# Kernel tuning notes

Measured on AMD Instinct MI355X. Metric: run time of the kernel, lower is better.

The kernel has to match this reference:

```python
import jax, jax.numpy as jnp
import numpy as np

S, D, DD, REL, R = 4096, 128, 64, 8, 512
FC_IN = DD * (REL * S + R)  # 2,129,920


def setup_inputs() -> dict:
    key = jax.random.key(0)
    ks = jax.random.split(key, 7)
    return {
        "inputs": jax.random.randint(ks[0], (S,), 0, 2, dtype=jnp.int32),
        "rule_features": jax.random.normal(ks[1], (DD, R), dtype=jnp.float32),
        "embed_w": jax.random.normal(ks[2], (S, D), dtype=jnp.float32),
        "rel_w": jax.random.normal(ks[3], (REL, D), dtype=jnp.float32),
        "dise_w": jax.random.normal(ks[4], (DD, D), dtype=jnp.float32),
        "fc_w": jax.random.normal(ks[5], (DD, FC_IN), dtype=jnp.float32) * 0.01,
        "fc_b": jax.random.normal(ks[6], (DD,), dtype=jnp.float32),
    }


def reference(inputs, rule_features, embed_w, rel_w, dise_w, fc_w, fc_b):
    eps = 1e-6
    dt = embed_w.dtype
    # mask rows where the symptom indicator is nonzero (original builds mask
    # row-by-row with torch.nonzero; equivalent to broadcasting inputs != 0)
    mask = (inputs != 0).astype(dt)                                  # [S]
    # (embed + rel) * mask  -> [S, REL, D] -> [S*REL, D]
    x = (embed_w[:, None, :] + rel_w[None, :, :]) * mask[:, None, None]
    x = x.reshape(-1, embed_w.shape[-1])                             # [N, D]
    # cosine similarity of every disease embedding vs every (sym,rel) vector
    sq = jnp.sum(x * x, axis=1)                                      # [N]
    xn = jnp.where(sq > 0, jnp.sqrt(jnp.where(sq > 0, sq, 1.0)), 0.0)
    dn = jnp.sqrt(jnp.sum(dise_w * dise_w, axis=1))                  # [DD]
    dots = jnp.einsum('kd,nd->kn', dise_w, x)                        # [DD, N]
    kg = dots / jnp.maximum(dn[:, None] * xn[None, :], eps)          # [DD, N]
    hidden = jnp.concatenate([rule_features, kg], axis=1).reshape(1, -1)
    out = jax.nn.sigmoid(hidden @ fc_w.T + fc_b)                     # [1, DD]
    return out
```

## Files before the change

### kernel.cpp

```cpp
#include <hip/hip_runtime.h>
#include <math.h>

namespace {
constexpr int S_N   = 4096;
constexpr int D_N   = 128;
constexpr int DD_N  = 64;
constexpr int REL_N = 8;
constexpr int R_N   = 512;
constexpr int NTOT  = S_N * REL_N;
constexpr int ROWLEN = R_N + NTOT;
constexpr long long FC_IN_N = (long long)DD_N * ROWLEN;
constexpr int NCH   = 32;
constexpr int CHUNK2 = (int)(FC_IN_N / NCH);
constexpr int NF4   = CHUNK2 / 4;
constexpr int RPB   = 8;
constexpr int KG_N  = DD_N / RPB;
constexpr int NBLK3 = NCH * KG_N;
constexpr int SEP   = 132;
typedef float floatx4 __attribute__((ext_vector_type(4)));

__device__ __forceinline__ float dot4(const float4& a, const float4& b) {
    return a.x*b.x + a.y*b.y + a.z*b.z + a.w*b.w;
}
}

__global__ __launch_bounds__(256) void k_pre(const int* __restrict__ inputs,
                                             const float* __restrict__ dise,
                                             const float* __restrict__ embed,
                                             const float* __restrict__ rel,
                                             float* __restrict__ DE,
                                             float* __restrict__ DR,
                                             float* __restrict__ dsc_g,
                                             float* __restrict__ xinv) {
    __shared__ float sd[DD_N * 129];
    __shared__ __align__(16) float se[16 * SEP];
    __shared__ __align__(16) float sr[REL_N * SEP];
    __shared__ float rr[REL_N];
    const int tid  = threadIdx.x;
    const int lane = tid & 63;
    const int wave = tid >> 6;
    const int s0   = blockIdx.x * 16;

    for (int i = tid; i < DD_N * D_N; i += 256)
        sd[(i >> 7) * 129 + (i & 127)] = dise[i];
    for (int i = tid; i < 16 * 32; i += 256) {
        const int row = i >> 5, col = i & 31;
        *reinterpret_cast<float4*>(&se[row * SEP + col * 4]) =
            reinterpret_cast<const float4*>(embed + (size_t)s0 * D_N)[i];
    }
    if (tid < REL_N * 32) {
        const int row = tid >> 5, col = tid & 31;
        *reinterpret_cast<float4*>(&sr[row * SEP + col * 4]) =
            reinterpret_cast<const float4*>(rel)[tid];
    }
    __syncthreads();

    if (tid < REL_N) {
        float a = 0.f;
        for (int e = 0; e < D_N; ++e) { float v = sr[tid * SEP + e]; a += v * v; }
        rr[tid] = a;
    }

    float dw[D_N];
    float dsq = 0.f;
    #pragma unroll
    for (int e = 0; e < D_N; ++e) {
        dw[e] = sd[lane * 129 + e];
        dsq += dw[e] * dw[e];
    }
    const float dsc = rsqrtf(dsq);

    if (blockIdx.x == 0) {
        if (wave == 0) dsc_g[lane] = dsc;
        #pragma unroll
        for (int rr2 = 0; rr2 < 2; ++rr2) {
            const int r = wave * 2 + rr2;
            float a = 0.f;
            #pragma unroll
            for (int e = 0; e < D_N; ++e) a += dw[e] * sr[r * SEP + e];
            DR[lane * REL_N + r] = a;
        }
    }

    {
        float4 o;
        float* op = reinterpret_cast<float*>(&o);
        #pragma unroll
        for (int jj = 0; jj < 4; ++jj) {
            const int nl = wave * 4 + jj;
            const float4* xr = reinterpret_cast<const float4*>(&se[nl * SEP]);
            float a0 = 0.f, a1 = 0.f, a2 = 0.f, a3 = 0.f;
            #pragma unroll
            for (int i = 0; i < 32; i += 4) {
                float4 x0 = xr[i], x1 = xr[i + 1], x2 = xr[i + 2], x3 = xr[i + 3];
                a0 += dw[4*i+ 0]*x0.x + dw[4*i+ 1]*x0.y + dw[4*i+ 2]*x0.z + dw[4*i+ 3]*x0.w;
                a1 += dw[4*i+ 4]*x1.x + dw[4*i+ 5]*x1.y + dw[4*i+ 6]*x1.z + dw[4*i+ 7]*x1.w;
                a2 += dw[4*i+ 8]*x2.x + dw[4*i+ 9]*x2.y + dw[4*i+10]*x2.z + dw[4*i+11]*x2.w;
                a3 += dw[4*i+12]*x3.x + dw[4*i+13]*x3.y + dw[4*i+14]*x3.z + dw[4*i+15]*x3.w;
            }
            op[jj] = a0 + a1 + a2 + a3;
        }
        *reinterpret_cast<float4*>(DE + (size_t)lane * S_N + s0 + wave * 4) = o;
    }

    __syncthreads();

    if (tid < 128) {
        const int sl = tid >> 3, r = tid & 7;
        const float4* ev4 = reinterpret_cast<const float4*>(&se[sl * SEP]);
        const float4* rv4 = reinterpret_cast<const float4*>(&sr[r * SEP]);
        float ee = 0.f, er = 0.f;
        #pragma unroll
        for (int i = 0; i < 32; ++i) {
            float4 ev = ev4[i], rv = rv4[i];
            ee += dot4(ev, ev);
            er += dot4(ev, rv);
        }
        const float sq = ee + 2.f * er + rr[r];
        const bool m = (inputs[s0 + sl] != 0);
        xinv[(size_t)(s0 + sl) * REL_N + r] = (m && sq > 0.f) ? rsqrtf(sq) : 0.f;
    }
}

__global__ __launch_bounds__(256) void k_kg2(const float* __restrict__ rf,
                                             const float* __restrict__ DE,
                                             const float* __restrict__ DR,
                                             const float* __restrict__ dsc_g,
                                             const float* __restrict__ xinv,
                                             float* __restrict__ h) {
    __shared__ __align__(16) float sx[8192];
    __shared__ float sD[1024];
    const int tid = threadIdx.x;
    const int dd  = blockIdx.x >> 2;
    const int q   = blockIdx.x & 3;
    const int n0  = q * 8192;
    const int s0  = q * 1024;

    for (int i = tid; i < 2048; i += 256)
        reinterpret_cast<float4*>(sx)[i] = reinterpret_cast<const float4*>(xinv + n0)[i];
    if (tid < 256)
        reinterpret_cast<float4*>(sD)[tid] =
            reinterpret_cast<const float4*>(DE + (size_t)dd * S_N + s0)[tid];
    const float dsc = dsc_g[dd];
    const float4 drlo = reinterpret_cast<const float4*>(DR + dd * REL_N)[0];
    const float4 drhi = reinterpret_cast<const float4*>(DR + dd * REL_N)[1];
    const float4 drv = (tid & 1) ? drhi : drlo;
    __syncthreads();

    float* hb = h + (size_t)dd * ROWLEN + R_N + n0;
    #pragma unroll
    for (int i = 0; i < 8; ++i) {
        const int f4i = i * 256 + tid;
        const int ln  = f4i * 4;
        const float de = sD[f4i >> 1];
        float4 xv = reinterpret_cast<const float4*>(sx)[f4i];
        float4 o;
        o.x = dsc * xv.x * (de + drv.x);
        o.y = dsc * xv.y * (de + drv.y);
        o.z = dsc * xv.z * (de + drv.z);
        o.w = dsc * xv.w * (de + drv.w);
        *reinterpret_cast<float4*>(hb + ln) = o;
    }
    if (q == 0 && tid < 128)
        reinterpret_cast<float4*>(h + (size_t)dd * ROWLEN)[tid] =
            reinterpret_cast<const float4*>(rf + (size_t)dd * R_N)[tid];
}

__global__ __launch_bounds__(512, 1) void k_mv(const float* __restrict__ fcw,
                                               const float* __restrict__ h,
                                               float* __restrict__ partials) {
    const int tid = threadIdx.x;
    const int swz = (blockIdx.x & 7) * (NBLK3 / 8) + (blockIdx.x >> 3);
    const int c  = swz >> 3;
    const int kg = swz & 7;

    const float4* hp = reinterpret_cast<const float4*>(h) + (size_t)c * NF4;
    const floatx4* wp = reinterpret_cast<const floatx4*>(fcw)
                        + (size_t)(kg * RPB) * (FC_IN_N / 4) + (size_t)c * NF4;

    float acc[RPB];
    #pragma unroll
    for (int j = 0; j < RPB; ++j) acc[j] = 0.f;

    #pragma unroll 2
    for (int i = 0; i < 32; ++i) {
        const int idx = i * 512 + tid;
        float4 hv = hp[idx];
        #pragma unroll
        for (int j = 0; j < RPB; ++j) {
            floatx4 w = __builtin_nontemporal_load(wp + (size_t)j * (FC_IN_N / 4) + idx);
            acc[j] += w.x * hv.x + w.y * hv.y + w.z * hv.z + w.w * hv.w;
        }
    }
    if (tid < 256) {
        const int idx = 32 * 512 + tid;
        float4 hv = hp[idx];
        #pragma unroll
        for (int j = 0; j < RPB; ++j) {
            floatx4 w = __builtin_nontemporal_load(wp + (size_t)j * (FC_IN_N / 4) + idx);
            acc[j] += w.x * hv.x + w.y * hv.y + w.z * hv.z + w.w * hv.w;
        }
    }

    #pragma unroll
    for (int m = 32; m >= 1; m >>= 1) {
        #pragma unroll
        for (int j = 0; j < RPB; ++j) acc[j] += __shfl_xor(acc[j], m);
    }
    __shared__ float red[8][RPB];
    if ((tid & 63) == 0) {
        const int wv = tid >> 6;
        #pragma unroll
        for (int j = 0; j < RPB; ++j) red[wv][j] = acc[j];
    }
    __syncthreads();
    if (tid < RPB) {
        float s = 0.f;
        #pragma unroll
        for (int wv = 0; wv < 8; ++wv) s += red[wv][tid];
        partials[(size_t)swz * RPB + tid] = s;
    }
}

__global__ __launch_bounds__(256) void k_fin(const float* __restrict__ partials,
                                             const float* __restrict__ fcb,
                                             float* __restrict__ out) {
    const int tid = threadIdx.x;
    const int k = tid & 63, g = tid >> 6;
    float s = 0.f;
    for (int b = g; b < NCH; b += 4) s += partials[(size_t)b * 64 + k];
    __shared__ float red[4][64];
    red[g][k] = s;
    __syncthreads();
    if (tid < 64) {
        float t = red[0][tid] + red[1][tid] + red[2][tid] + red[3][tid] + fcb[tid];
        out[tid] = 1.0f / (1.0f + expf(-t));
    }
}

extern "C" void kernel_launch(void* const* d_in, const int* in_sizes, int n_in,
                              void* d_out, int out_size, void* d_ws, size_t ws_size,
                              hipStream_t stream) {
    const int*   inputs = (const int*)  d_in[0];
    const float* rf     = (const float*)d_in[1];
    const float* embed  = (const float*)d_in[2];
    const float* rel    = (const float*)d_in[3];
    const float* dise   = (const float*)d_in[4];
    const float* fcw    = (const float*)d_in[5];
    const float* fcb    = (const float*)d_in[6];
    float* out = (float*)d_out;

    float* ws = (float*)d_ws;
    float* h        = ws;
    float* partials = h + FC_IN_N;
    float* DE       = partials + NCH * 64;
    float* DR       = DE + (size_t)DD_N * S_N;
    float* dsc_g    = DR + DD_N * REL_N;
    float* xinv     = dsc_g + 64;

    hipLaunchKernelGGL(k_pre,  dim3(S_N / 16), dim3(256), 0, stream,
                       inputs, dise, embed, rel, DE, DR, dsc_g, xinv);
    hipLaunchKernelGGL(k_kg2,  dim3(DD_N * 4), dim3(256), 0, stream, rf, DE, DR, dsc_g, xinv, h);
    hipLaunchKernelGGL(k_mv,   dim3(NBLK3),    dim3(512), 0, stream, fcw, h, partials);
    hipLaunchKernelGGL(k_fin,  dim3(1),        dim3(256), 0, stream, partials, fcb, out);
}
```

Before: 112.1 us.

## Fuse final reduction into matvec via last-block atomic counter; drop nontemporal loads

Removes the separate single-block finalize kernel. Each matvec block now writes its partials, fences, and bumps a global counter, and the last block to finish sums the partials, adds the bias and applies the sigmoid. The counter is reset in the first kernel. The fc weight loads also switch from nontemporal builtins to plain float4 loads, which changes cache behaviour on the dominant weight stream. The goal is to save one kernel launch, at the cost of an atomic and fences in every block.

After: 134.7 us, median of 2. 1.2x slower.

```diff
diff --git a/kernel.cpp b/kernel.cpp
--- a/kernel.cpp
+++ b/kernel.cpp
@@ -31,7 +31,8 @@
                                              float* __restrict__ DE,
                                              float* __restrict__ DR,
                                              float* __restrict__ dsc_g,
-                                             float* __restrict__ xinv) {
+                                             float* __restrict__ xinv,
+                                             int* __restrict__ counter) {
     __shared__ float sd[DD_N * 129];
     __shared__ __align__(16) float se[16 * SEP];
     __shared__ __align__(16) float sr[REL_N * SEP];
@@ -40,6 +41,8 @@
     const int lane = tid & 63;
     const int wave = tid >> 6;
     const int s0   = blockIdx.x * 16;
+
+    if (blockIdx.x == 0 && tid == 0) *counter = 0;
 
     for (int i = tid; i < DD_N * D_N; i += 256)
         sd[(i >> 7) * 129 + (i & 127)] = dise[i];
@@ -168,14 +171,17 @@
 
 __global__ __launch_bounds__(512, 1) void k_mv(const float* __restrict__ fcw,
                                                const float* __restrict__ h,
-                                               float* __restrict__ partials) {
+                                               float* __restrict__ partials,
+                                               const float* __restrict__ fcb,
+                                               float* __restrict__ out,
+                                               int* __restrict__ counter) {
     const int tid = threadIdx.x;
     const int swz = (blockIdx.x & 7) * (NBLK3 / 8) + (blockIdx.x >> 3);
     const int c  = swz >> 3;
     const int kg = swz & 7;
 
     const float4* hp = reinterpret_cast<const float4*>(h) + (size_t)c * NF4;
-    const floatx4* wp = reinterpret_cast<const floatx4*>(fcw)
+    const float4* wp = reinterpret_cast<const float4*>(fcw)
                         + (size_t)(kg * RPB) * (FC_IN_N / 4) + (size_t)c * NF4;
 
     float acc[RPB];
@@ -188,7 +194,7 @@
         float4 hv = hp[idx];
         #pragma unroll
         for (int j = 0; j < RPB; ++j) {
-            floatx4 w = __builtin_nontemporal_load(wp + (size_t)j * (FC_IN_N / 4) + idx);
+            float4 w = wp[(size_t)j * (FC_IN_N / 4) + idx];
             acc[j] += w.x * hv.x + w.y * hv.y + w.z * hv.z + w.w * hv.w;
         }
     }
@@ -197,7 +203,7 @@
         float4 hv = hp[idx];
         #pragma unroll
         for (int j = 0; j < RPB; ++j) {
-            floatx4 w = __builtin_nontemporal_load(wp + (size_t)j * (FC_IN_N / 4) + idx);
+            float4 w = wp[(size_t)j * (FC_IN_N / 4) + idx];
             acc[j] += w.x * hv.x + w.y * hv.y + w.z * hv.z + w.w * hv.w;
         }
     }
@@ -214,27 +220,28 @@
         for (int j = 0; j < RPB; ++j) red[wv][j] = acc[j];
     }
     __syncthreads();
-    if (tid < RPB) {
-        float s = 0.f;
-        #pragma unroll
-        for (int wv = 0; wv < 8; ++wv) s += red[wv][tid];
-        partials[(size_t)swz * RPB + tid] = s;
-    }
-}
-
-__global__ __launch_bounds__(256) void k_fin(const float* __restrict__ partials,
-                                             const float* __restrict__ fcb,
-                                             float* __restrict__ out) {
-    const int tid = threadIdx.x;
-    const int k = tid & 63, g = tid >> 6;
-    float s = 0.f;
-    for (int b = g; b < NCH; b += 4) s += partials[(size_t)b * 64 + k];
-    __shared__ float red[4][64];
-    red[g][k] = s;
-    __syncthreads();
-    if (tid < 64) {
-        float t = red[0][tid] + red[1][tid] + red[2][tid] + red[3][tid] + fcb[tid];
-        out[tid] = 1.0f / (1.0f + expf(-t));
+
+    __shared__ bool amLast;
+    if (tid == 0) {
+        #pragma unroll
+        for (int j = 0; j < RPB; ++j) {
+            float s = 0.f;
+            #pragma unroll
+            for (int wv = 0; wv < 8; ++wv) s += red[wv][j];
+            partials[(size_t)swz * RPB + j] = s;
+        }
+        __threadfence();
+        amLast = (atomicAdd(counter, 1) == NBLK3 - 1);
+    }
+    __syncthreads();
+
+    if (amLast) {
+        __threadfence();
+        if (tid < DD_N) {
+            float t = fcb[tid];
+            for (int cc = 0; cc < NCH; ++cc) t += partials[(size_t)cc * DD_N + tid];
+            out[tid] = 1.0f / (1.0f + expf(-t));
+        }
     }
 }
 
@@ -257,10 +264,11 @@
     float* DR       = DE + (size_t)DD_N * S_N;
     float* dsc_g    = DR + DD_N * REL_N;
     float* xinv     = dsc_g + 64;
+    int*   counter  = (int*)(xinv + NTOT);
 
     hipLaunchKernelGGL(k_pre,  dim3(S_N / 16), dim3(256), 0, stream,
-                       inputs, dise, embed, rel, DE, DR, dsc_g, xinv);
+                       inputs, dise, embed, rel, DE, DR, dsc_g, xinv, counter);
     hipLaunchKernelGGL(k_kg2,  dim3(DD_N * 4), dim3(256), 0, stream, rf, DE, DR, dsc_g, xinv, h);
-    hipLaunchKernelGGL(k_mv,   dim3(NBLK3),    dim3(512), 0, stream, fcw, h, partials);
-    hipLaunchKernelGGL(k_fin,  dim3(1),        dim3(256), 0, stream, partials, fcb, out);
-}
+    hipLaunchKernelGGL(k_mv,   dim3(NBLK3),    dim3(512), 0, stream,
+                       fcw, h, partials, fcb, out, counter);
+}
```

## Fuse hidden-vector construction into the matvec kernel and drop the h buffer

Applied to the files above, without the earlier changes.

Removes the k_kg2 kernel that materialized the 2.1M-float hidden vector h in workspace. k_mv now rebuilds each hidden chunk on the fly from rule_features, DE, DR, dsc and xinv while streaming fc_w, with each chunk covering exactly two disease rows. This saves the write and re-read of about 8.5MB plus one kernel launch. In exchange, the hidden values are recomputed by all 8 row-group blocks that share a chunk, which adds ALU work and small cached reads inside the bandwidth-bound loop.

Result: faster. 103.6 us (-7.5%).

```diff
diff --git a/kernel.cpp b/kernel.cpp
--- a/kernel.cpp
+++ b/kernel.cpp
@@ -122,83 +122,62 @@
     }
 }
 
-__global__ __launch_bounds__(256) void k_kg2(const float* __restrict__ rf,
-                                             const float* __restrict__ DE,
-                                             const float* __restrict__ DR,
-                                             const float* __restrict__ dsc_g,
-                                             const float* __restrict__ xinv,
-                                             float* __restrict__ h) {
-    __shared__ __align__(16) float sx[8192];
-    __shared__ float sD[1024];
-    const int tid = threadIdx.x;
-    const int dd  = blockIdx.x >> 2;
-    const int q   = blockIdx.x & 3;
-    const int n0  = q * 8192;
-    const int s0  = q * 1024;
-
-    for (int i = tid; i < 2048; i += 256)
-        reinterpret_cast<float4*>(sx)[i] = reinterpret_cast<const float4*>(xinv + n0)[i];
-    if (tid < 256)
-        reinterpret_cast<float4*>(sD)[tid] =
-            reinterpret_cast<const float4*>(DE + (size_t)dd * S_N + s0)[tid];
-    const float dsc = dsc_g[dd];
-    const float4 drlo = reinterpret_cast<const float4*>(DR + dd * REL_N)[0];
-    const float4 drhi = reinterpret_cast<const float4*>(DR + dd * REL_N)[1];
-    const float4 drv = (tid & 1) ? drhi : drlo;
-    __syncthreads();
-
-    float* hb = h + (size_t)dd * ROWLEN + R_N + n0;
-    #pragma unroll
-    for (int i = 0; i < 8; ++i) {
-        const int f4i = i * 256 + tid;
-        const int ln  = f4i * 4;
-        const float de = sD[f4i >> 1];
-        float4 xv = reinterpret_cast<const float4*>(sx)[f4i];
-        float4 o;
-        o.x = dsc * xv.x * (de + drv.x);
-        o.y = dsc * xv.y * (de + drv.y);
-        o.z = dsc * xv.z * (de + drv.z);
-        o.w = dsc * xv.w * (de + drv.w);
-        *reinterpret_cast<float4*>(hb + ln) = o;
-    }
-    if (q == 0 && tid < 128)
-        reinterpret_cast<float4*>(h + (size_t)dd * ROWLEN)[tid] =
-            reinterpret_cast<const float4*>(rf + (size_t)dd * R_N)[tid];
-}
-
 __global__ __launch_bounds__(512, 1) void k_mv(const float* __restrict__ fcw,
-                                               const float* __restrict__ h,
+                                               const float* __restrict__ rf,
+                                               const float* __restrict__ DE,
+                                               const float* __restrict__ DR,
+                                               const float* __restrict__ dsc_g,
+                                               const float* __restrict__ xinv,
                                                float* __restrict__ partials) {
     const int tid = threadIdx.x;
     const int swz = (blockIdx.x & 7) * (NBLK3 / 8) + (blockIdx.x >> 3);
     const int c  = swz >> 3;
     const int kg = swz & 7;
 
-    const float4* hp = reinterpret_cast<const float4*>(h) + (size_t)c * NF4;
     const floatx4* wp = reinterpret_cast<const floatx4*>(fcw)
                         + (size_t)(kg * RPB) * (FC_IN_N / 4) + (size_t)c * NF4;
+    const float4* xv4 = reinterpret_cast<const float4*>(xinv);
 
     float acc[RPB];
     #pragma unroll
     for (int j = 0; j < RPB; ++j) acc[j] = 0.f;
 
-    #pragma unroll 2
-    for (int i = 0; i < 32; ++i) {
-        const int idx = i * 512 + tid;
-        float4 hv = hp[idx];
-        #pragma unroll
-        for (int j = 0; j < RPB; ++j) {
-            floatx4 w = __builtin_nontemporal_load(wp + (size_t)j * (FC_IN_N / 4) + idx);
-            acc[j] += w.x * hv.x + w.y * hv.y + w.z * hv.z + w.w * hv.w;
-        }
-    }
-    if (tid < 256) {
-        const int idx = 32 * 512 + tid;
-        float4 hv = hp[idx];
-        #pragma unroll
-        for (int j = 0; j < RPB; ++j) {
-            floatx4 w = __builtin_nontemporal_load(wp + (size_t)j * (FC_IN_N / 4) + idx);
-            acc[j] += w.x * hv.x + w.y * hv.y + w.z * hv.z + w.w * hv.w;
+    #pragma unroll
+    for (int half = 0; half < 2; ++half) {
+        const int dd = 2 * c + half;
+        const float dscv = dsc_g[dd];
+        const float4 drlo = reinterpret_cast<const float4*>(DR)[dd * 2];
+        const float4 drhi = reinterpret_cast<const float4*>(DR)[dd * 2 + 1];
+        const float4 drv = (tid & 1) ? drhi : drlo;
+        const float* DEp = DE + (size_t)dd * S_N;
+        const int wbase = half * (ROWLEN / 4);
+
+        if (tid < 128) {
+            float4 hv = reinterpret_cast<const float4*>(rf)[dd * 128 + tid];
+            const int idx = wbase + tid;
+            #pragma unroll
+            for (int j = 0; j < RPB; ++j) {
+                floatx4 w = __builtin_nontemporal_load(wp + (size_t)j * (FC_IN_N / 4) + idx);
+                acc[j] += w.x * hv.x + w.y * hv.y + w.z * hv.z + w.w * hv.w;
+            }
+        }
+
+        #pragma unroll 2
+        for (int i = 0; i < 16; ++i) {
+            const int col4k = i * 512 + tid;
+            const int idx = wbase + 128 + col4k;
+            const float de = DEp[col4k >> 1];
+            const float4 xv = xv4[col4k];
+            float4 hv;
+            hv.x = dscv * xv.x * (de + drv.x);
+            hv.y = dscv * xv.y * (de + drv.y);
+            hv.z = dscv * xv.z * (de + drv.z);
+            hv.w = dscv * xv.w * (de + drv.w);
+            #pragma unroll
+            for (int j = 0; j < RPB; ++j) {
+                floatx4 w = __builtin_nontemporal_load(wp + (size_t)j * (FC_IN_N / 4) + idx);
+                acc[j] += w.x * hv.x + w.y * hv.y + w.z * hv.z + w.w * hv.w;
+            }
         }
     }
 
@@ -251,16 +230,15 @@
     float* out = (float*)d_out;
 
     float* ws = (float*)d_ws;
-    float* h        = ws;
-    float* partials = h + FC_IN_N;
+    float* partials = ws;
     float* DE       = partials + NCH * 64;
     float* DR       = DE + (size_t)DD_N * S_N;
     float* dsc_g    = DR + DD_N * REL_N;
     float* xinv     = dsc_g + 64;
 
-    hipLaunchKernelGGL(k_pre,  dim3(S_N / 16), dim3(256), 0, stream,
+    hipLaunchKernelGGL(k_pre, dim3(S_N / 16), dim3(256), 0, stream,
                        inputs, dise, embed, rel, DE, DR, dsc_g, xinv);
-    hipLaunchKernelGGL(k_kg2,  dim3(DD_N * 4), dim3(256), 0, stream, rf, DE, DR, dsc_g, xinv, h);
-    hipLaunchKernelGGL(k_mv,   dim3(NBLK3),    dim3(512), 0, stream, fcw, h, partials);
-    hipLaunchKernelGGL(k_fin,  dim3(1),        dim3(256), 0, stream, partials, fcb, out);
-}
+    hipLaunchKernelGGL(k_mv,  dim3(NBLK3),    dim3(512), 0, stream,
+                       fcw, rf, DE, DR, dsc_g, xinv, partials);
+    hipLaunchKernelGGL(k_fin, dim3(1),        dim3(256), 0, stream, partials, fcb, out);
+}
```
